# Kernel tuning notes

Measured on AMD Instinct MI355X. Metric: run time of the kernel, lower is better.

## Reference

```python
import jax, jax.numpy as jnp
import numpy as np

B, T, D, H = 2, 2048, 1024, 16
DH = D // H  # 64


def setup_inputs() -> dict:
    key = jax.random.key(0)
    k1, k2, k3 = jax.random.split(key, 3)
    x = jax.random.normal(k1, (B, T, D), dtype=jnp.float32)
    # torch nn.Linear(d, 3d, bias=False): y = x @ W.T; we store W already transposed as [in, out]
    Wqkv = jax.random.normal(k2, (D, 3 * D), dtype=jnp.float32) * (1.0 / np.sqrt(D))
    Wproj = jax.random.normal(k3, (D, D), dtype=jnp.float32) * (1.0 / np.sqrt(D))
    return {"x": x, "Wqkv": Wqkv, "Wproj": Wproj}


def reference(x, Wqkv, Wproj):
    Bx, Tx, C = x.shape
    qkv = x @ Wqkv                                   # [B,T,3C]
    q, k, v = jnp.split(qkv, 3, axis=-1)
    def rs(t):
        return t.reshape(Bx, Tx, H, DH).transpose(0, 2, 1, 3)  # [B,H,T,DH]
    q, k, v = rs(q), rs(k), rs(v)
    scale = 1.0 / jnp.sqrt(jnp.asarray(DH, dtype=x.dtype))
    att = jnp.einsum('bhqd,bhkd->bhqk', q, k) * scale          # [B,H,T,T]
    causal = jnp.tril(jnp.ones((Tx, Tx), dtype=bool))
    att = jnp.where(causal[None, None, :, :], att, jnp.asarray(-jnp.inf, dtype=att.dtype))
    att = jax.nn.softmax(att, axis=-1)
    out = jnp.einsum('bhqk,bhkd->bhqd', att, v)                # [B,H,T,DH]
    out = out.transpose(0, 2, 1, 3).reshape(Bx, Tx, C)         # [B,T,C]
    return out @ Wproj
```

## Files before the change

kernel.cpp:

```cpp
#include <hip/hip_runtime.h>
#include <hip/hip_bf16.h>

#define BB 2
#define TT 2048
#define DD 1024
#define HH 16
#define MM (BB*TT)
#define N3 (3*DD)
#define QKW 2048

typedef __attribute__((ext_vector_type(8))) short short8;
typedef __attribute__((ext_vector_type(4))) float f32x4;
typedef __attribute__((ext_vector_type(16))) float f32x16;

#define ZERO16 (f32x16){0,0,0,0,0,0,0,0,0,0,0,0,0,0,0,0}

#define GLDS16(g, l) __builtin_amdgcn_global_load_lds( \
    (const __attribute__((address_space(1))) void*)(g), \
    (__attribute__((address_space(3))) void*)(l), 16, 0, 0)

__device__ __forceinline__ unsigned short f2bf(float f) {
    union { float f; unsigned u; } v; v.f = f;
    unsigned r = v.u + 0x7FFFu + ((v.u >> 16) & 1u);
    return (unsigned short)(r >> 16);
}

__device__ __forceinline__ unsigned cvt_pk_bf16(float lo, float hi) {
    unsigned r;
    asm("v_cvt_pk_bf16_f32 %0, %1, %2" : "=v"(r) : "v"(lo), "v"(hi));
    return r;
}

__device__ __forceinline__ float fast_exp2(float x) {
    float r;
    asm("v_exp_f32 %0, %1" : "=v"(r) : "v"(x));
    return r;
}
__device__ __forceinline__ float fast_rcp(float x) {
    float r;
    asm("v_rcp_f32 %0, %1" : "=v"(r) : "v"(x));
    return r;
}

__global__ void prep_kernel(const float* __restrict__ x,
                            const float* __restrict__ Wqkv,
                            const float* __restrict__ Wproj,
                            unsigned short* __restrict__ xb,
                            unsigned short* __restrict__ wqkvt,
                            unsigned short* __restrict__ wprojt) {
    __shared__ float tile[32][33];
    const int bid = blockIdx.x;
    const int tx = threadIdx.x, ty = threadIdx.y;
    if (bid < 4096) {
        const float* src;
        unsigned short* dst;
        int rows, cols, c0, r0;
        if (bid < 3072) {
            src = Wqkv; dst = wqkvt; rows = DD; cols = N3;
            c0 = (bid % 96) * 32; r0 = (bid / 96) * 32;
        } else {
            src = Wproj; dst = wprojt; rows = DD; cols = DD;
            int b2 = bid - 3072;
            c0 = (b2 & 31) * 32; r0 = (b2 >> 5) * 32;
        }
#pragma unroll
        for (int i = 0; i < 4; i++) {
            int r = ty + i * 8;
            tile[r][tx] = src[(size_t)(r0 + r) * cols + c0 + tx];
        }
        __syncthreads();
#pragma unroll
        for (int i = 0; i < 4; i++) {
            int r = ty + i * 8;
            dst[(size_t)(c0 + r) * rows + r0 + tx] = f2bf(tile[tx][r]);
        }
    } else {
        const int t = ty * 32 + tx;
        int i = (bid - 4096) * 256 + t;
#pragma unroll
        for (int k = 0; k < 2; k++, i += 262144) {
            const float4* s = reinterpret_cast<const float4*>(x) + (size_t)i * 2;
            float4 a = s[0], b = s[1];
            unsigned short r[8] = {f2bf(a.x), f2bf(a.y), f2bf(a.z), f2bf(a.w),
                                   f2bf(b.x), f2bf(b.y), f2bf(b.z), f2bf(b.w)};
            *reinterpret_cast<uint4*>(xb + (size_t)i * 8) = *reinterpret_cast<uint4*>(r);
        }
    }
}

__global__ __launch_bounds__(512, 2)
void gemm256_qkv(const unsigned short* __restrict__ A,
                 const unsigned short* __restrict__ Bt,
                 unsigned short* __restrict__ qkv2,
                 unsigned short* __restrict__ Vout,
                 float scale) {
    __shared__ unsigned short Al[2][2][128][64];
    __shared__ unsigned short Bl[2][192][64];

    const int id = blockIdx.y * 16 + blockIdx.x;
    const int swzid = (id & 7) * 32 + (id >> 3);
    const int tm = (swzid >> 4) * 256, tn = (swzid & 15) * 192;
    const int t = threadIdx.x, w = t >> 6, l = t & 63;
    const int wm = w >> 2, wn = w & 3;
    const int lo = l & 15, hi = l >> 4;
    const int srow = l >> 3;
    const int sg = (l & 7) ^ srow;

    f32x4 acc[8][3];
#pragma unroll
    for (int i = 0; i < 8; i++)
#pragma unroll
        for (int j = 0; j < 3; j++) acc[i][j] = (f32x4){0.f, 0.f, 0.f, 0.f};

    const unsigned short* Abase = A + (size_t)(tm + w * 16 + srow) * 1024 + sg * 8;
    const unsigned short* Bbase = Bt + (size_t)(tn + w * 24 + srow) * 1024 + sg * 8;

#define STG_A(KT, H) { \
    GLDS16(Abase + (size_t)(H) * 128 * 1024 + ((KT) & 15) * 64, &Al[(KT) & 1][H][w * 16][0]); \
    GLDS16(Abase + (size_t)(H) * 128 * 1024 + 8 * 1024 + ((KT) & 15) * 64, &Al[(KT) & 1][H][w * 16 + 8][0]); }
#define STG_B(KT) { \
    GLDS16(Bbase + ((KT) & 15) * 64, &Bl[(KT) & 1][w * 24][0]); \
    GLDS16(Bbase + (size_t)8 * 1024 + ((KT) & 15) * 64, &Bl[(KT) & 1][w * 24 + 8][0]); \
    GLDS16(Bbase + (size_t)16 * 1024 + ((KT) & 15) * 64, &Bl[(KT) & 1][w * 24 + 16][0]); }

#define LOAD_A(AFR, KP, MH) { \
    const char* ab = (const char*)&Al[KP][wm][0][0]; \
    _Pragma("unroll") \
    for (int fi = 0; fi < 4; fi++) \
    _Pragma("unroll") \
    for (int ks = 0; ks < 2; ks++) \
        AFR[fi][ks] = *reinterpret_cast<const short8*>( \
            ab + ((MH) * 64 + fi * 16 + lo) * 128 + (((ks * 4 + hi) ^ (lo & 7)) << 4)); }
#define LOAD_B(BFR, KP) { \
    const char* bb = (const char*)&Bl[KP][0][0]; \
    _Pragma("unroll") \
    for (int fj = 0; fj < 3; fj++) \
    _Pragma("unroll") \
    for (int ks = 0; ks < 2; ks++) \
        BFR[fj][ks] = *reinterpret_cast<const short8*>( \
            bb + (wn * 48 + fj * 16 + lo) * 128 + (((ks * 4 + hi) ^ (lo & 7)) << 4)); }

#define MFMA24(MH, AFR, BFR) { \
    _Pragma("unroll") \
    for (int ks = 0; ks < 2; ks++) \
    _Pragma("unroll") \
    for (int fi = 0; fi < 4; fi++) \
    _Pragma("unroll") \
    for (int fj = 0; fj < 3; fj++) \
        acc[(MH) * 4 + fi][fj] = __builtin_amdgcn_mfma_f32_16x16x32_bf16( \
            AFR[fi][ks], BFR[fj][ks], acc[(MH) * 4 + fi][fj], 0, 0, 0); }

#define BAR __builtin_amdgcn_s_barrier()
#define LGKM0 asm volatile("s_waitcnt lgkmcnt(0)")
#define SP1 __builtin_amdgcn_s_setprio(1)
#define SP0 __builtin_amdgcn_s_setprio(0)

    STG_A(0, 0); STG_A(0, 1); STG_B(0); STG_B(1);
    asm volatile("s_waitcnt vmcnt(3)");
    BAR;

    for (int i = 0; i < 8; i++) {
        const int kt = 2 * i;
        short8 AF[4][2], BF[3][2];
        LOAD_A(AF, 0, 0); LOAD_B(BF, 0);
        STG_A(kt + 1, 0); STG_A(kt + 1, 1);
        BAR; LGKM0; SP1; MFMA24(0, AF, BF); SP0; BAR;
        LOAD_A(AF, 0, 1);
        STG_B(kt + 2);
        BAR; LGKM0; SP1; MFMA24(1, AF, BF); SP0;
        asm volatile("s_waitcnt vmcnt(3)");
        BAR;
        LOAD_A(AF, 1, 0); LOAD_B(BF, 1);
        STG_A(kt + 2, 0); STG_A(kt + 2, 1);
        BAR; LGKM0; SP1; MFMA24(0, AF, BF); SP0; BAR;
        LOAD_A(AF, 1, 1);
        STG_B(kt + 3);
        BAR; LGKM0; SP1; MFMA24(1, AF, BF); SP0;
        asm volatile("s_waitcnt vmcnt(3)");
        BAR;
    }

#pragma unroll
    for (int i = 0; i < 8; i++)
#pragma unroll
        for (int j = 0; j < 3; j++) {
            const int col = tn + wn * 48 + j * 16 + lo;
            const int row0 = tm + wm * 128 + i * 16 + hi * 4;
            if (col < 2 * DD) {
                float s = (col < DD) ? scale : 1.0f;
#pragma unroll
                for (int r = 0; r < 4; r++)
                    qkv2[(size_t)(row0 + r) * QKW + col] = f2bf(acc[i][j][r] * s);
            } else {
                unsigned short pk[4];
#pragma unroll
                for (int r = 0; r < 4; r++) pk[r] = f2bf(acc[i][j][r]);
                *reinterpret_cast<uint2*>(&Vout[(size_t)(col - 2 * DD) * MM + row0]) =
                    *reinterpret_cast<uint2*>(pk);
            }
        }
#undef STG_A
#undef STG_B
#undef LOAD_A
#undef LOAD_B
#undef MFMA24
#undef BAR
#undef LGKM0
#undef SP1
#undef SP0
}

__global__ __launch_bounds__(256)
void gemm_proj(const unsigned short* __restrict__ A,
               const unsigned short* __restrict__ Bt,
               float* __restrict__ Cout) {
    __shared__ unsigned short As[128][64];
    __shared__ unsigned short Bs[64][64];
    const int nbx = 16;
    const int id = blockIdx.y * nbx + blockIdx.x;
    const int cpx = 512 >> 3;
    const int swz = (id & 7) * cpx + (id >> 3);
    const int tm = (swz / nbx) * 128, tn = (swz % nbx) * 64;
    const int t = threadIdx.x;
    const int w = t >> 6, lane = t & 63, lo = lane & 15, hi = lane >> 4;
    const int wr = w >> 1, wc = w & 1;

    f32x4 acc[4][2];
#pragma unroll
    for (int i = 0; i < 4; i++)
#pragma unroll
        for (int j = 0; j < 2; j++) acc[i][j] = (f32x4){0.f, 0.f, 0.f, 0.f};

    const int sr8 = lane >> 3;
    const int scol = (lane & 7) * 8;
    const unsigned short* ga = &A[(size_t)(tm + w * 32 + sr8) * 1024 + scol];
    const unsigned short* gb = &Bt[(size_t)(tn + w * 16 + sr8) * 1024 + scol];

    for (int k0 = 0; k0 < 1024; k0 += 64) {
        __syncthreads();
#pragma unroll
        for (int i = 0; i < 4; i++)
            GLDS16(ga + (size_t)(i * 8) * 1024 + k0, &As[w * 32 + i * 8][0]);
#pragma unroll
        for (int i = 0; i < 2; i++)
            GLDS16(gb + (size_t)(i * 8) * 1024 + k0, &Bs[w * 16 + i * 8][0]);
        __syncthreads();

        short8 af[4][2], bf[2][2];
#pragma unroll
        for (int i = 0; i < 4; i++)
#pragma unroll
            for (int ks = 0; ks < 2; ks++)
                af[i][ks] = *reinterpret_cast<const short8*>(&As[wr * 64 + i * 16 + lo][ks * 32 + hi * 8]);
#pragma unroll
        for (int j = 0; j < 2; j++)
#pragma unroll
            for (int ks = 0; ks < 2; ks++)
                bf[j][ks] = *reinterpret_cast<const short8*>(&Bs[wc * 32 + j * 16 + lo][ks * 32 + hi * 8]);
#pragma unroll
        for (int ks = 0; ks < 2; ks++)
#pragma unroll
            for (int i = 0; i < 4; i++)
#pragma unroll
                for (int j = 0; j < 2; j++)
                    acc[i][j] = __builtin_amdgcn_mfma_f32_16x16x32_bf16(af[i][ks], bf[j][ks], acc[i][j], 0, 0, 0);
    }
#pragma unroll
    for (int i = 0; i < 4; i++)
#pragma unroll
        for (int j = 0; j < 2; j++) {
            const int col = tn + wc * 32 + j * 16 + lo;
            const int row0 = tm + wr * 64 + i * 16 + hi * 4;
#pragma unroll
            for (int r = 0; r < 4; r++)
                Cout[(size_t)(row0 + r) * DD + col] = acc[i][j][r];
        }
}

struct AttnState {
    f32x16 o0, o1, lD;
};

__device__ __forceinline__ void attn_full_tile(
        const char* kbase, const char* vbase, const short8* bq, short8 ones1,
        AttnState& st, int sw4, int ql, int hi8, bool domask, int kvb, int qg) {
    short8 ak0[4], ak1[4];
#pragma unroll
    for (int ks = 0; ks < 4; ks++) {
        ak0[ks] = *reinterpret_cast<const short8*>(kbase + ql * 128 + (((ks * 2 + hi8) << 4) ^ sw4));
        ak1[ks] = *reinterpret_cast<const short8*>(kbase + (32 + ql) * 128 + (((ks * 2 + hi8) << 4) ^ sw4));
    }
    f32x16 sa0 = ZERO16, sa1 = ZERO16;
    __builtin_amdgcn_s_setprio(1);
#pragma unroll
    for (int ks = 0; ks < 4; ks++) {
        sa0 = __builtin_amdgcn_mfma_f32_32x32x16_bf16(ak0[ks], bq[ks], sa0, 0, 0, 0);
        sa1 = __builtin_amdgcn_mfma_f32_32x32x16_bf16(ak1[ks], bq[ks], sa1, 0, 0, 0);
    }
    __builtin_amdgcn_s_setprio(0);
    if (domask) {
#pragma unroll
        for (int r = 0; r < 16; r++) {
            int crow = (r & 3) + 8 * (r >> 2) + 4 * hi8;
            if (kvb + crow > qg) sa0[r] = -1e30f;
            if (kvb + 32 + crow > qg) sa1[r] = -1e30f;
        }
    }
#pragma unroll
    for (int r = 0; r < 16; r++) sa0[r] = fast_exp2(sa0[r]);
#pragma unroll
    for (int r = 0; r < 16; r++) sa1[r] = fast_exp2(sa1[r]);

    unsigned a01 = cvt_pk_bf16(sa0[0], sa0[1]),  a23 = cvt_pk_bf16(sa0[2], sa0[3]);
    unsigned a45 = cvt_pk_bf16(sa0[4], sa0[5]),  a67 = cvt_pk_bf16(sa0[6], sa0[7]);
    asm("v_permlane32_swap_b32 %0, %1" : "+v"(a01), "+v"(a45));
    asm("v_permlane32_swap_b32 %0, %1" : "+v"(a23), "+v"(a67));
    unsigned b01 = cvt_pk_bf16(sa0[8], sa0[9]),  b23 = cvt_pk_bf16(sa0[10], sa0[11]);
    unsigned b45 = cvt_pk_bf16(sa0[12], sa0[13]), b67 = cvt_pk_bf16(sa0[14], sa0[15]);
    asm("v_permlane32_swap_b32 %0, %1" : "+v"(b01), "+v"(b45));
    asm("v_permlane32_swap_b32 %0, %1" : "+v"(b23), "+v"(b67));
    unsigned c01 = cvt_pk_bf16(sa1[0], sa1[1]),  c23 = cvt_pk_bf16(sa1[2], sa1[3]);
    unsigned c45 = cvt_pk_bf16(sa1[4], sa1[5]),  c67 = cvt_pk_bf16(sa1[6], sa1[7]);
    asm("v_permlane32_swap_b32 %0, %1" : "+v"(c01), "+v"(c45));
    asm("v_permlane32_swap_b32 %0, %1" : "+v"(c23), "+v"(c67));
    unsigned d01 = cvt_pk_bf16(sa1[8], sa1[9]),  d23 = cvt_pk_bf16(sa1[10], sa1[11]);
    unsigned d45 = cvt_pk_bf16(sa1[12], sa1[13]), d67 = cvt_pk_bf16(sa1[14], sa1[15]);
    asm("v_permlane32_swap_b32 %0, %1" : "+v"(d01), "+v"(d45));
    asm("v_permlane32_swap_b32 %0, %1" : "+v"(d23), "+v"(d67));
    union { unsigned u[4]; short8 s; } f0s0, f1s0, f0s1, f1s1;
    f0s0.u[0] = a01; f0s0.u[1] = a23; f0s0.u[2] = a45; f0s0.u[3] = a67;
    f1s0.u[0] = b01; f1s0.u[1] = b23; f1s0.u[2] = b45; f1s0.u[3] = b67;
    f0s1.u[0] = c01; f0s1.u[1] = c23; f0s1.u[2] = c45; f0s1.u[3] = c67;
    f1s1.u[0] = d01; f1s1.u[1] = d23; f1s1.u[2] = d45; f1s1.u[3] = d67;

    short8 bv00 = *reinterpret_cast<const short8*>(vbase + ql * 128 + (((0 + hi8) << 4) ^ sw4));
    short8 bv01 = *reinterpret_cast<const short8*>(vbase + ql * 128 + (((2 + hi8) << 4) ^ sw4));
    short8 bv02 = *reinterpret_cast<const short8*>(vbase + ql * 128 + (((4 + hi8) << 4) ^ sw4));
    short8 bv03 = *reinterpret_cast<const short8*>(vbase + ql * 128 + (((6 + hi8) << 4) ^ sw4));
    short8 bv10 = *reinterpret_cast<const short8*>(vbase + (32 + ql) * 128 + (((0 + hi8) << 4) ^ sw4));
    short8 bv11 = *reinterpret_cast<const short8*>(vbase + (32 + ql) * 128 + (((2 + hi8) << 4) ^ sw4));
    short8 bv12 = *reinterpret_cast<const short8*>(vbase + (32 + ql) * 128 + (((4 + hi8) << 4) ^ sw4));
    short8 bv13 = *reinterpret_cast<const short8*>(vbase + (32 + ql) * 128 + (((6 + hi8) << 4) ^ sw4));
    __builtin_amdgcn_s_setprio(1);
    st.lD = __builtin_amdgcn_mfma_f32_32x32x16_bf16(f0s0.s, ones1, st.lD, 0, 0, 0);
    st.lD = __builtin_amdgcn_mfma_f32_32x32x16_bf16(f1s0.s, ones1, st.lD, 0, 0, 0);
    st.lD = __builtin_amdgcn_mfma_f32_32x32x16_bf16(f0s1.s, ones1, st.lD, 0, 0, 0);
    st.lD = __builtin_amdgcn_mfma_f32_32x32x16_bf16(f1s1.s, ones1, st.lD, 0, 0, 0);
    st.o0 = __builtin_amdgcn_mfma_f32_32x32x16_bf16(f0s0.s, bv00, st.o0, 0, 0, 0);
    st.o1 = __builtin_amdgcn_mfma_f32_32x32x16_bf16(f0s0.s, bv10, st.o1, 0, 0, 0);
    st.o0 = __builtin_amdgcn_mfma_f32_32x32x16_bf16(f1s0.s, bv01, st.o0, 0, 0, 0);
    st.o1 = __builtin_amdgcn_mfma_f32_32x32x16_bf16(f1s0.s, bv11, st.o1, 0, 0, 0);
    st.o0 = __builtin_amdgcn_mfma_f32_32x32x16_bf16(f0s1.s, bv02, st.o0, 0, 0, 0);
    st.o1 = __builtin_amdgcn_mfma_f32_32x32x16_bf16(f0s1.s, bv12, st.o1, 0, 0, 0);
    st.o0 = __builtin_amdgcn_mfma_f32_32x32x16_bf16(f1s1.s, bv03, st.o0, 0, 0, 0);
    st.o1 = __builtin_amdgcn_mfma_f32_32x32x16_bf16(f1s1.s, bv13, st.o1, 0, 0, 0);
    __builtin_amdgcn_s_setprio(0);
}

__device__ __forceinline__ void attn_half_tile(
        const char* kbase, const char* vbase, const short8* bq, short8 ones1,
        AttnState& st, int sw4, int ql, int hi8, int sub, int kvb, int qg) {
    short8 ak[4];
#pragma unroll
    for (int ks = 0; ks < 4; ks++)
        ak[ks] = *reinterpret_cast<const short8*>(
            kbase + (sub * 32 + ql) * 128 + (((ks * 2 + hi8) << 4) ^ sw4));
    f32x16 sa = ZERO16;
#pragma unroll
    for (int ks = 0; ks < 4; ks++)
        sa = __builtin_amdgcn_mfma_f32_32x32x16_bf16(ak[ks], bq[ks], sa, 0, 0, 0);

#pragma unroll
    for (int r = 0; r < 16; r++) {
        int crow = (r & 3) + 8 * (r >> 2) + 4 * hi8;
        if (kvb + sub * 32 + crow > qg) sa[r] = -1e30f;
    }
#pragma unroll
    for (int r = 0; r < 16; r++) sa[r] = fast_exp2(sa[r]);

    unsigned a01 = cvt_pk_bf16(sa[0], sa[1]),  a23 = cvt_pk_bf16(sa[2], sa[3]);
    unsigned a45 = cvt_pk_bf16(sa[4], sa[5]),  a67 = cvt_pk_bf16(sa[6], sa[7]);
    asm("v_permlane32_swap_b32 %0, %1" : "+v"(a01), "+v"(a45));
    asm("v_permlane32_swap_b32 %0, %1" : "+v"(a23), "+v"(a67));
    unsigned b01 = cvt_pk_bf16(sa[8], sa[9]),  b23 = cvt_pk_bf16(sa[10], sa[11]);
    unsigned b45 = cvt_pk_bf16(sa[12], sa[13]), b67 = cvt_pk_bf16(sa[14], sa[15]);
    asm("v_permlane32_swap_b32 %0, %1" : "+v"(b01), "+v"(b45));
    asm("v_permlane32_swap_b32 %0, %1" : "+v"(b23), "+v"(b67));
    union { unsigned u[4]; short8 s; } f0, f1;
    f0.u[0] = a01; f0.u[1] = a23; f0.u[2] = a45; f0.u[3] = a67;
    f1.u[0] = b01; f1.u[1] = b23; f1.u[2] = b45; f1.u[3] = b67;

    st.lD = __builtin_amdgcn_mfma_f32_32x32x16_bf16(f0.s, ones1, st.lD, 0, 0, 0);
    st.lD = __builtin_amdgcn_mfma_f32_32x32x16_bf16(f1.s, ones1, st.lD, 0, 0, 0);

    short8 bv00 = *reinterpret_cast<const short8*>(vbase + ql * 128 + (((sub * 4 + 0 + hi8) << 4) ^ sw4));
    short8 bv01 = *reinterpret_cast<const short8*>(vbase + ql * 128 + (((sub * 4 + 2 + hi8) << 4) ^ sw4));
    short8 bv10 = *reinterpret_cast<const short8*>(vbase + (32 + ql) * 128 + (((sub * 4 + 0 + hi8) << 4) ^ sw4));
    short8 bv11 = *reinterpret_cast<const short8*>(vbase + (32 + ql) * 128 + (((sub * 4 + 2 + hi8) << 4) ^ sw4));
    st.o0 = __builtin_amdgcn_mfma_f32_32x32x16_bf16(f0.s, bv00, st.o0, 0, 0, 0);
    st.o1 = __builtin_amdgcn_mfma_f32_32x32x16_bf16(f0.s, bv10, st.o1, 0, 0, 0);
    st.o0 = __builtin_amdgcn_mfma_f32_32x32x16_bf16(f1.s, bv01, st.o0, 0, 0, 0);
    st.o1 = __builtin_amdgcn_mfma_f32_32x32x16_bf16(f1.s, bv11, st.o1, 0, 0, 0);
}

__global__ __launch_bounds__(256)
void attn_kernel(const unsigned short* __restrict__ qkv2,
                 const unsigned short* __restrict__ vtg,
                 unsigned short* __restrict__ outp) {
    __shared__ unsigned short Ks[4][64][64];
    __shared__ unsigned short Vt[4][64][64];

    const int b = blockIdx.z, h = blockIdx.x, p = blockIdx.y;
    const int qcl = p, qch = 31 - p;
    const int L = p + 1, Hn = 32 - p;
    const int NSTEP = 17;
    const int t = threadIdx.x;
    const int w = t >> 6, l = t & 63, ql = l & 31, hi8 = l >> 5;
    const int pr = w >> 1, rg = w & 1;
    const int q0h = qch * 64 + rg * 32;
    const int q0l = qcl * 64 + rg * 32;
    const int q0p = pr ? q0l : q0h;
    const unsigned short* base2 = qkv2 + (size_t)b * TT * QKW;

    short8 bq[4];
#pragma unroll
    for (int ks = 0; ks < 4; ks++)
        bq[ks] = *reinterpret_cast<const short8*>(
            &base2[(size_t)(q0p + ql) * QKW + h * 64 + ks * 16 + hi8 * 8]);

    AttnState st;
    st.o0 = ZERO16; st.o1 = ZERO16; st.lD = ZERO16;

    short8 ones1;
#pragma unroll
    for (int j = 0; j < 8; j++) ones1[j] = (short)0x3F80;

    const int krow = l >> 3;
    const int kc8 = (l & 7) ^ krow;
    const unsigned short* gk = &base2[(size_t)(w * 8 + krow) * QKW + DD + h * 64 + kc8 * 8];
    const unsigned short* gv = &vtg[(size_t)(h * 64 + w * 8 + krow) * MM + b * TT + kc8 * 8];

#define STAGE(TI) { \
    const int _s = (TI) & 3; \
    const size_t _kb = (size_t)(TI) * 64; \
    GLDS16(gk + _kb * QKW, &Ks[_s][w * 8][0]); \
    GLDS16(gk + (_kb + 32) * QKW, &Ks[_s][32 + w * 8][0]); \
    GLDS16(gv + _kb, &Vt[_s][w * 8][0]); \
    GLDS16(gv + (size_t)32 * MM + _kb, &Vt[_s][32 + w * 8][0]); }

#define WRITE_OUT(Q0) { \
    _Pragma("unroll") \
    for (int r = 0; r < 16; r++) { \
        int src = (r & 3) + 8 * (r >> 2) + 4 * hi8; \
        float inv = fast_rcp(st.lD[r]); \
        size_t off = (size_t)(b * TT + (Q0) + src) * DD + h * 64 + ql; \
        outp[off] = f2bf(st.o0[r] * inv); \
        outp[off + 32] = f2bf(st.o1[r] * inv); \
    } }

    STAGE(0);
    int nIss = 1;
    __syncthreads();

    const int sw4 = (ql & 7) << 4;
    for (int s = 0; s < NSTEP; s++) {
        {
            const int sn = s + 1;
            int lastN;
            if (sn < L) lastN = sn;
            else if (sn < NSTEP - 1) lastN = L + 2 * (sn - L) + 1;
            else if (sn == NSTEP - 1) lastN = Hn - 1;
            else lastN = -1;
            while (nIss <= lastN) { STAGE(nIss); nIss++; }
        }

        if (s == L && pr == 1) {
            WRITE_OUT(q0l);
            st.o0 = ZERO16; st.o1 = ZERO16; st.lD = ZERO16;
#pragma unroll
            for (int ks = 0; ks < 4; ks++)
                bq[ks] = *reinterpret_cast<const short8*>(
                    &base2[(size_t)(q0h + ql) * QKW + h * 64 + ks * 16 + hi8 * 8]);
        }

        if (s < L) {
            const int tile = s;
            const char* kbase = (const char*)&Ks[tile & 3][0][0];
            const char* vbase = (const char*)&Vt[tile & 3][0][0];
            const bool domask = (pr == 1) && (s == L - 1);
            attn_full_tile(kbase, vbase, bq, ones1, st, sw4, ql, hi8,
                           domask, tile * 64, q0p + ql);
        } else if (s < NSTEP - 1) {
            const int tile = L + 2 * (s - L) + pr;
            const char* kbase = (const char*)&Ks[tile & 3][0][0];
            const char* vbase = (const char*)&Vt[tile & 3][0][0];
            attn_full_tile(kbase, vbase, bq, ones1, st, sw4, ql, hi8,
                           false, 0, 0);
        } else {
            const int tile = Hn - 1;
            const char* kbase = (const char*)&Ks[tile & 3][0][0];
            const char* vbase = (const char*)&Vt[tile & 3][0][0];
            attn_half_tile(kbase, vbase, bq, ones1, st, sw4, ql, hi8,
                           pr, tile * 64, q0h + ql);
        }
        __syncthreads();
    }

    float* xf = (float*)&Ks[0][0][0];
    float* xl = (float*)&Vt[0][0][0];
    const int tid128 = (w & 1) * 64 + l;
    if (pr == 1) {
#pragma unroll
        for (int r = 0; r < 16; r++) {
            xf[r * 128 + tid128] = st.o0[r];
            xf[(16 + r) * 128 + tid128] = st.o1[r];
            xl[r * 128 + tid128] = st.lD[r];
        }
    }
    __syncthreads();
    if (pr == 0) {
#pragma unroll
        for (int r = 0; r < 16; r++) {
            st.o0[r] += xf[r * 128 + tid128];
            st.o1[r] += xf[(16 + r) * 128 + tid128];
            st.lD[r] += xl[r * 128 + tid128];
        }
        WRITE_OUT(q0h);
    }
#undef STAGE
#undef WRITE_OUT
}

extern "C" void kernel_launch(void* const* d_in, const int* in_sizes, int n_in,
                              void* d_out, int out_size, void* d_ws, size_t ws_size,
                              hipStream_t stream) {
    const float* x     = (const float*)d_in[0];
    const float* Wqkv  = (const float*)d_in[1];
    const float* Wproj = (const float*)d_in[2];
    float* out = (float*)d_out;

    unsigned short* xb     = (unsigned short*)d_ws;
    unsigned short* wqkvt  = xb + (size_t)MM * DD;
    unsigned short* wprojt = wqkvt + (size_t)N3 * DD;
    unsigned short* qkv2   = wprojt + (size_t)DD * DD;
    unsigned short* vtg    = qkv2 + (size_t)MM * QKW;
    unsigned short* attout = vtg + (size_t)DD * MM;
    size_t need = ((size_t)MM * DD + (size_t)N3 * DD + (size_t)DD * DD +
                   (size_t)MM * QKW + (size_t)DD * MM + (size_t)MM * DD) * 2;
    if (ws_size < need) return;

    const float sc = 0.125f * 1.44269504088896f;

    prep_kernel<<<5120, dim3(32, 8), 0, stream>>>(x, Wqkv, Wproj, xb, wqkvt, wprojt);

    gemm256_qkv<<<dim3(16, 16), 512, 0, stream>>>(xb, wqkvt, qkv2, vtg, sc);

    attn_kernel<<<dim3(HH, 16, BB), 256, 0, stream>>>(qkv2, vtg, attout);

    gemm_proj<<<dim3(16, 32), 256, 0, stream>>>(attout, wprojt, out);
}
```

Measured before the change: 100.8 us.

## Load attention K/V fragments directly from global memory instead of LDS staging

Removes the four-slot LDS ring buffer for K and V tiles, the async global_load_lds staging and the per-step __syncthreads. Each wave now reads its K and V MFMA operands straight from global memory (qkv2 and the transposed V), and V loads are hoisted ahead of the QK^T MFMAs. LDS is kept only for the final cross-wave reduction. This cuts barrier and LDS traffic and may raise occupancy, but every wave re-reads K/V from global/L2 and loses the prefetch pipelining, so latency may be exposed.

```diff
diff --git a/kernel.cpp b/kernel.cpp
--- a/kernel.cpp
+++ b/kernel.cpp
@@ -281,15 +281,30 @@
     f32x16 o0, o1, lD;
 };
 
-__device__ __forceinline__ void attn_full_tile(
-        const char* kbase, const char* vbase, const short8* bq, short8 ones1,
-        AttnState& st, int sw4, int ql, int hi8, bool domask, int kvb, int qg) {
+__device__ __forceinline__ void attn_tile_g(
+        const unsigned short* __restrict__ kbase,
+        const unsigned short* __restrict__ vbase,
+        const short8* bq, short8 ones1, AttnState& st,
+        int ql, int hi8, bool domask, int kvb, int qg) {
+    const unsigned short* kr0 = kbase + (size_t)ql * QKW + hi8 * 8;
+    const unsigned short* kr1 = kbase + (size_t)(32 + ql) * QKW + hi8 * 8;
     short8 ak0[4], ak1[4];
 #pragma unroll
     for (int ks = 0; ks < 4; ks++) {
-        ak0[ks] = *reinterpret_cast<const short8*>(kbase + ql * 128 + (((ks * 2 + hi8) << 4) ^ sw4));
-        ak1[ks] = *reinterpret_cast<const short8*>(kbase + (32 + ql) * 128 + (((ks * 2 + hi8) << 4) ^ sw4));
-    }
+        ak0[ks] = *reinterpret_cast<const short8*>(kr0 + ks * 16);
+        ak1[ks] = *reinterpret_cast<const short8*>(kr1 + ks * 16);
+    }
+    const unsigned short* vr0 = vbase + (size_t)ql * MM + hi8 * 8;
+    const unsigned short* vr1 = vbase + (size_t)(32 + ql) * MM + hi8 * 8;
+    short8 bv00 = *reinterpret_cast<const short8*>(vr0);
+    short8 bv01 = *reinterpret_cast<const short8*>(vr0 + 16);
+    short8 bv02 = *reinterpret_cast<const short8*>(vr0 + 32);
+    short8 bv03 = *reinterpret_cast<const short8*>(vr0 + 48);
+    short8 bv10 = *reinterpret_cast<const short8*>(vr1);
+    short8 bv11 = *reinterpret_cast<const short8*>(vr1 + 16);
+    short8 bv12 = *reinterpret_cast<const short8*>(vr1 + 32);
+    short8 bv13 = *reinterpret_cast<const short8*>(vr1 + 48);
+
     f32x16 sa0 = ZERO16, sa1 = ZERO16;
     __builtin_amdgcn_s_setprio(1);
 #pragma unroll
@@ -333,14 +348,6 @@
     f0s1.u[0] = c01; f0s1.u[1] = c23; f0s1.u[2] = c45; f0s1.u[3] = c67;
     f1s1.u[0] = d01; f1s1.u[1] = d23; f1s1.u[2] = d45; f1s1.u[3] = d67;
 
-    short8 bv00 = *reinterpret_cast<const short8*>(vbase + ql * 128 + (((0 + hi8) << 4) ^ sw4));
-    short8 bv01 = *reinterpret_cast<const short8*>(vbase + ql * 128 + (((2 + hi8) << 4) ^ sw4));
-    short8 bv02 = *reinterpret_cast<const short8*>(vbase + ql * 128 + (((4 + hi8) << 4) ^ sw4));
-    short8 bv03 = *reinterpret_cast<const short8*>(vbase + ql * 128 + (((6 + hi8) << 4) ^ sw4));
-    short8 bv10 = *reinterpret_cast<const short8*>(vbase + (32 + ql) * 128 + (((0 + hi8) << 4) ^ sw4));
-    short8 bv11 = *reinterpret_cast<const short8*>(vbase + (32 + ql) * 128 + (((2 + hi8) << 4) ^ sw4));
-    short8 bv12 = *reinterpret_cast<const short8*>(vbase + (32 + ql) * 128 + (((4 + hi8) << 4) ^ sw4));
-    short8 bv13 = *reinterpret_cast<const short8*>(vbase + (32 + ql) * 128 + (((6 + hi8) << 4) ^ sw4));
     __builtin_amdgcn_s_setprio(1);
     st.lD = __builtin_amdgcn_mfma_f32_32x32x16_bf16(f0s0.s, ones1, st.lD, 0, 0, 0);
     st.lD = __builtin_amdgcn_mfma_f32_32x32x16_bf16(f1s0.s, ones1, st.lD, 0, 0, 0);
@@ -357,14 +364,23 @@
     __builtin_amdgcn_s_setprio(0);
 }
 
-__device__ __forceinline__ void attn_half_tile(
-        const char* kbase, const char* vbase, const short8* bq, short8 ones1,
-        AttnState& st, int sw4, int ql, int hi8, int sub, int kvb, int qg) {
+__device__ __forceinline__ void attn_half_g(
+        const unsigned short* __restrict__ kbase,
+        const unsigned short* __restrict__ vbase,
+        const short8* bq, short8 ones1, AttnState& st,
+        int ql, int hi8, int sub, int kvb, int qg) {
+    const unsigned short* kr = kbase + (size_t)(sub * 32 + ql) * QKW + hi8 * 8;
     short8 ak[4];
 #pragma unroll
     for (int ks = 0; ks < 4; ks++)
-        ak[ks] = *reinterpret_cast<const short8*>(
-            kbase + (sub * 32 + ql) * 128 + (((ks * 2 + hi8) << 4) ^ sw4));
+        ak[ks] = *reinterpret_cast<const short8*>(kr + ks * 16);
+    const unsigned short* vr0 = vbase + (size_t)ql * MM + sub * 32 + hi8 * 8;
+    const unsigned short* vr1 = vbase + (size_t)(32 + ql) * MM + sub * 32 + hi8 * 8;
+    short8 bv00 = *reinterpret_cast<const short8*>(vr0);
+    short8 bv01 = *reinterpret_cast<const short8*>(vr0 + 16);
+    short8 bv10 = *reinterpret_cast<const short8*>(vr1);
+    short8 bv11 = *reinterpret_cast<const short8*>(vr1 + 16);
+
     f32x16 sa = ZERO16;
 #pragma unroll
     for (int ks = 0; ks < 4; ks++)
@@ -392,11 +408,6 @@
 
     st.lD = __builtin_amdgcn_mfma_f32_32x32x16_bf16(f0.s, ones1, st.lD, 0, 0, 0);
     st.lD = __builtin_amdgcn_mfma_f32_32x32x16_bf16(f1.s, ones1, st.lD, 0, 0, 0);
-
-    short8 bv00 = *reinterpret_cast<const short8*>(vbase + ql * 128 + (((sub * 4 + 0 + hi8) << 4) ^ sw4));
-    short8 bv01 = *reinterpret_cast<const short8*>(vbase + ql * 128 + (((sub * 4 + 2 + hi8) << 4) ^ sw4));
-    short8 bv10 = *reinterpret_cast<const short8*>(vbase + (32 + ql) * 128 + (((sub * 4 + 0 + hi8) << 4) ^ sw4));
-    short8 bv11 = *reinterpret_cast<const short8*>(vbase + (32 + ql) * 128 + (((sub * 4 + 2 + hi8) << 4) ^ sw4));
     st.o0 = __builtin_amdgcn_mfma_f32_32x32x16_bf16(f0.s, bv00, st.o0, 0, 0, 0);
     st.o1 = __builtin_amdgcn_mfma_f32_32x32x16_bf16(f0.s, bv10, st.o1, 0, 0, 0);
     st.o0 = __builtin_amdgcn_mfma_f32_32x32x16_bf16(f1.s, bv01, st.o0, 0, 0, 0);
@@ -407,8 +418,8 @@
 void attn_kernel(const unsigned short* __restrict__ qkv2,
                  const unsigned short* __restrict__ vtg,
                  unsigned short* __restrict__ outp) {
-    __shared__ unsigned short Ks[4][64][64];
-    __shared__ unsigned short Vt[4][64][64];
+    __shared__ float xf[32 * 128];
+    __shared__ float xl[16 * 128];
 
     const int b = blockIdx.z, h = blockIdx.x, p = blockIdx.y;
     const int qcl = p, qch = 31 - p;
@@ -421,6 +432,8 @@
     const int q0l = qcl * 64 + rg * 32;
     const int q0p = pr ? q0l : q0h;
     const unsigned short* base2 = qkv2 + (size_t)b * TT * QKW;
+    const unsigned short* kb0 = base2 + DD + h * 64;
+    const unsigned short* vb0 = vtg + (size_t)(h * 64) * MM + b * TT;
 
     short8 bq[4];
 #pragma unroll
@@ -434,19 +447,6 @@
     short8 ones1;
 #pragma unroll
     for (int j = 0; j < 8; j++) ones1[j] = (short)0x3F80;
-
-    const int krow = l >> 3;
-    const int kc8 = (l & 7) ^ krow;
-    const unsigned short* gk = &base2[(size_t)(w * 8 + krow) * QKW + DD + h * 64 + kc8 * 8];
-    const unsigned short* gv = &vtg[(size_t)(h * 64 + w * 8 + krow) * MM + b * TT + kc8 * 8];
-
-#define STAGE(TI) { \
-    const int _s = (TI) & 3; \
-    const size_t _kb = (size_t)(TI) * 64; \
-    GLDS16(gk + _kb * QKW, &Ks[_s][w * 8][0]); \
-    GLDS16(gk + (_kb + 32) * QKW, &Ks[_s][32 + w * 8][0]); \
-    GLDS16(gv + _kb, &Vt[_s][w * 8][0]); \
-    GLDS16(gv + (size_t)32 * MM + _kb, &Vt[_s][32 + w * 8][0]); }
 
 #define WRITE_OUT(Q0) { \
     _Pragma("unroll") \
@@ -458,22 +458,7 @@
         outp[off + 32] = f2bf(st.o1[r] * inv); \
     } }
 
-    STAGE(0);
-    int nIss = 1;
-    __syncthreads();
-
-    const int sw4 = (ql & 7) << 4;
     for (int s = 0; s < NSTEP; s++) {
-        {
-            const int sn = s + 1;
-            int lastN;
-            if (sn < L) lastN = sn;
-            else if (sn < NSTEP - 1) lastN = L + 2 * (sn - L) + 1;
-            else if (sn == NSTEP - 1) lastN = Hn - 1;
-            else lastN = -1;
-            while (nIss <= lastN) { STAGE(nIss); nIss++; }
-        }
-
         if (s == L && pr == 1) {
             WRITE_OUT(q0l);
             st.o0 = ZERO16; st.o1 = ZERO16; st.lD = ZERO16;
@@ -485,29 +470,20 @@
 
         if (s < L) {
             const int tile = s;
-            const char* kbase = (const char*)&Ks[tile & 3][0][0];
-            const char* vbase = (const char*)&Vt[tile & 3][0][0];
             const bool domask = (pr == 1) && (s == L - 1);
-            attn_full_tile(kbase, vbase, bq, ones1, st, sw4, ql, hi8,
-                           domask, tile * 64, q0p + ql);
+            attn_tile_g(kb0 + (size_t)tile * 64 * QKW, vb0 + tile * 64,
+                        bq, ones1, st, ql, hi8, domask, tile * 64, q0p + ql);
         } else if (s < NSTEP - 1) {
             const int tile = L + 2 * (s - L) + pr;
-            const char* kbase = (const char*)&Ks[tile & 3][0][0];
-            const char* vbase = (const char*)&Vt[tile & 3][0][0];
-            attn_full_tile(kbase, vbase, bq, ones1, st, sw4, ql, hi8,
-                           false, 0, 0);
+            attn_tile_g(kb0 + (size_t)tile * 64 * QKW, vb0 + tile * 64,
+                        bq, ones1, st, ql, hi8, false, 0, 0);
         } else {
             const int tile = Hn - 1;
-            const char* kbase = (const char*)&Ks[tile & 3][0][0];
-            const char* vbase = (const char*)&Vt[tile & 3][0][0];
-            attn_half_tile(kbase, vbase, bq, ones1, st, sw4, ql, hi8,
-                           pr, tile * 64, q0h + ql);
-        }
-        __syncthreads();
-    }
-
-    float* xf = (float*)&Ks[0][0][0];
-    float* xl = (float*)&Vt[0][0][0];
+            attn_half_g(kb0 + (size_t)tile * 64 * QKW, vb0 + tile * 64,
+                        bq, ones1, st, ql, hi8, pr, tile * 64, q0h + ql);
+        }
+    }
+
     const int tid128 = (w & 1) * 64 + l;
     if (pr == 1) {
 #pragma unroll
@@ -527,7 +503,6 @@
         }
         WRITE_OUT(q0h);
     }
-#undef STAGE
 #undef WRITE_OUT
 }
 
```

Result: slower. 129.6 us (+28.6%).
